# Performance work log

Hardware: AMD Instinct MI355X
Metric: run time of the kernel (lower is better)

Reference implementation:

```python
import jax, jax.numpy as jnp
import numpy as np

EPS = 1e-12  # torch F.normalize eps


def setup_inputs() -> dict:
    key = jax.random.key(0)
    k1, k2, k3 = jax.random.split(key, 3)
    B, way, shot, D, H, W = 64, 5, 1, 640, 5, 5
    nq = 75
    base = jax.random.normal(k1, (B, way, shot, D, H, W), dtype=jnp.float32)
    query = jax.random.normal(k2, (B, nq, D, H, W), dtype=jnp.float32)
    r = jax.random.normal(k3, (2,), dtype=jnp.float32) * 0.1
    return {"base": base, "query": query, "r": r, "neighbor_k": 5}


def reference(base, query, r, neighbor_k):
    B, way, shot, D, H, W = base.shape
    nq = query.shape[1]
    hw = H * W

    # ---- global-cosine branch: spatial-mean descriptors ----
    base_mean = base.reshape(B, way * shot, D, hw).mean(axis=-1)   # [B, way*shot, D]
    query_mean = query.reshape(B, nq, D, hw).mean(axis=-1)         # [B, nq, D]
    bm = base_mean / jnp.maximum(jnp.linalg.norm(base_mean, axis=-1, keepdims=True), EPS)
    qm = query_mean / jnp.maximum(jnp.linalg.norm(query_mean, axis=-1, keepdims=True), EPS)
    logits = jnp.einsum('bqd,bkd->bqk', qm, bm)                    # [B, nq, way*shot]

    # ---- DN4 image-to-class branch (vectorized over the original triple loop) ----
    # query local descriptors: [B, nq, hw, D], L2-normalized over channels
    q = query.reshape(B, nq, D, hw).transpose(0, 1, 3, 2)
    q = q / jnp.linalg.norm(q, axis=-1, keepdims=True)
    # support local descriptors: base_mix [B, way, shot*D, hw], column-normalized
    s = base.reshape(B, way, shot * D, hw)
    s = s / jnp.linalg.norm(s, axis=2, keepdims=True)
    # cosine sims between every query patch and every support patch of each class
    # (requires shot*D == D, i.e. shot == 1, as in the original code)
    sim = jnp.einsum('bqpd,bkdl->bqkpl', q, s)                     # [B, nq, way, hw, hw]
    topk_vals, _ = jax.lax.top_k(sim, neighbor_k)                  # [B, nq, way, hw, k]
    logits_dn4 = topk_vals.sum(axis=(-1, -2)) / neighbor_k         # [B, nq, way]

    return r[0] * logits + r[1] * logits_dn4
```

## Files before the change

### kernel.cpp

```cpp
#include <hip/hip_runtime.h>
#include <hip/hip_bf16.h>
#include <math.h>

#define NB    64
#define WAY   5
#define DCH   640
#define HW    25
#define NQ    75
#define NBK   5
#define EPSN  1e-12f

#define NDG   (DCH / 8)
#define SCOLS 128
#define CD    160
#define NCHK  (DCH / CD)
#define DGC   (CD / 8)
#define CFL   (CD * HW)
#define CTS   132

typedef __attribute__((ext_vector_type(8)))  short  bf16x8;
typedef __attribute__((ext_vector_type(8)))  ushort u16x8;
typedef __attribute__((ext_vector_type(16))) float  f32x16;
typedef __attribute__((ext_vector_type(4)))  float  f32x4;

__device__ inline ushort f2bf(float f) {
    uint u = __float_as_uint(f);
    return (ushort)((u + 0x7FFFu + ((u >> 16) & 1u)) >> 16);
}

__global__ __launch_bounds__(256) void k_prep(const float* __restrict__ base,
                                              float* __restrict__ invs,
                                              float* __restrict__ invsm,
                                              ushort* __restrict__ sT)
{
    const int bk = blockIdx.x;
    const int b  = bk / WAY;
    const int k  = bk - b * WAY;
    const float* src = base + (size_t)bk * (DCH * HW);
    __shared__ float lds[DCH * HW];
    __shared__ float red[256];
    const int tid = threadIdx.x;

    const f32x4* s4 = (const f32x4*)src;
    f32x4* l4 = (f32x4*)lds;
    for (int i = tid; i < (DCH * HW) / 4; i += 256)
        l4[i] = __builtin_nontemporal_load(s4 + i);
    __syncthreads();

    if (tid < HW) {
        float ss = 0.f;
        for (int d = 0; d < DCH; ++d) { float v = lds[d * HW + tid]; ss = fmaf(v, v, ss); }
        invs[bk * HW + tid] = rsqrtf(ss);
    }

    float ssq = 0.f;
    for (int d = tid; d < DCH; d += 256) {
        float s = 0.f;
        #pragma unroll
        for (int pp = 0; pp < HW; ++pp) s += lds[d * HW + pp];
        float m = s * (1.0f / HW);
        ssq = fmaf(m, m, ssq);
    }
    red[tid] = ssq;
    __syncthreads();
    for (int s = 128; s > 0; s >>= 1) {
        if (tid < s) red[tid] += red[tid + s];
        __syncthreads();
    }
    if (tid == 0) invsm[bk] = 1.0f / fmaxf(sqrtf(red[0]), EPSN);

    ushort* dstb = sT + (size_t)b * (NDG * SCOLS * 8);
    for (int t = tid; t < NDG * HW; t += 256) {
        const int dg = t / HW, l = t - dg * HW;
        u16x8 v;
        #pragma unroll
        for (int e = 0; e < 8; ++e) v[e] = f2bf(lds[(dg * 8 + e) * HW + l]);
        *(u16x8*)&dstb[((size_t)dg * SCOLS + k * HW + l) * 8] = v;
    }
    if (k == 0) {
        const u16x8 z = (u16x8)(ushort)0;
        for (int t = tid; t < NDG * 3; t += 256) {
            const int dg = t / 3, sc = 125 + (t - dg * 3);
            *(u16x8*)&dstb[((size_t)dg * SCOLS + sc) * 8] = z;
        }
    }
}

__global__ __launch_bounds__(256, 4) void k_fused(const float* __restrict__ query,
                                                  const ushort* __restrict__ sT,
                                                  const float* __restrict__ invs,
                                                  const float* __restrict__ invsm,
                                                  const float* __restrict__ r,
                                                  float* __restrict__ out)
{
    __shared__ ushort s_bq[2][DGC * 32 * 8];
    __shared__ float invs_l[SCOLS];
    __shared__ float invsm_l[WAY];

    const int tid  = threadIdx.x;
    const int wid  = tid >> 6;
    const int lane = tid & 63;
    const int p    = lane & 31;
    const int hi   = lane >> 5;

    const int wk = (blockIdx.x & 7) * 600 + (blockIdx.x >> 3);
    const int b  = wk / NQ;
    const int q  = wk - b * NQ;

    if (tid < WAY * HW) invs_l[tid] = invs[b * WAY * HW + tid];
    if (tid >= WAY * HW && tid < SCOLS) invs_l[tid] = 0.f;
    if (tid < WAY)      invsm_l[tid] = invsm[b * WAY + tid];

    const float* qrow = query + (size_t)(b * NQ + q) * (DCH * HW);
    const ushort* sTb = sT + (size_t)b * (NDG * SCOLS * 8);

    f32x16 accT = {}, accG = {};
    f32x4 lA0 = {}, lA1 = {}, lA2 = {}, lA3 = {};
    f32x4 lB0 = {}, lB1 = {}, lB2 = {}, lB3 = {};

#define LOADQ(c, R0, R1, R2, R3)                                              \
    {                                                                         \
        const f32x4* s4_ = (const f32x4*)(qrow + (size_t)(c) * CFL);          \
        R0 = __builtin_nontemporal_load(s4_ + tid);                           \
        R1 = __builtin_nontemporal_load(s4_ + 256 + tid);                     \
        R2 = __builtin_nontemporal_load(s4_ + 512 + tid);                     \
        if (tid < 232) R3 = __builtin_nontemporal_load(s4_ + 768 + tid);      \
    }

#define WR4(DST, SLOT, V)                                                     \
    {                                                                         \
        _Pragma("unroll")                                                     \
        for (int j = 0; j < 4; ++j) {                                         \
            const int flat = (SLOT) * 4 + j;                                  \
            const int d  = flat / 25;                                         \
            const int pp = flat - d * 25;                                     \
            (DST)[((d >> 3) * 32 + pp) * 8 + (d & 7)] = f2bf((V)[j]);         \
        }                                                                     \
    }

#define WRITEQ(BUF, R0, R1, R2, R3)                                           \
    {                                                                         \
        ushort* db_ = &s_bq[BUF][0];                                          \
        WR4(db_, tid, R0)                                                     \
        WR4(db_, 256 + tid, R1)                                               \
        WR4(db_, 512 + tid, R2)                                               \
        if (tid < 232) WR4(db_, 768 + tid, R3)                                \
    }

#define COMPUTE(BUF, C)                                                       \
    {                                                                         \
        _Pragma("unroll")                                                     \
        for (int ks = 0; ks < DGC / 2; ++ks) {                                \
            const int dgl = ks * 2 + hi;                                      \
            const bf16x8 bq = *(const bf16x8*)&s_bq[BUF][(dgl * 32 + p) * 8]; \
            const bf16x8 a  = *(const bf16x8*)(sTb +                          \
                ((size_t)((C) * DGC + dgl) * SCOLS + wid * 32 + p) * 8);      \
            accT = __builtin_amdgcn_mfma_f32_32x32x16_bf16(a,  bq, accT, 0, 0, 0); \
            accG = __builtin_amdgcn_mfma_f32_32x32x16_bf16(bq, bq, accG, 0, 0, 0); \
        }                                                                     \
    }

    LOADQ(0, lA0, lA1, lA2, lA3)
    for (int i = tid; i < 2 * DGC * 7; i += 256) {
        const int bu = i / (DGC * 7), r2 = i % (DGC * 7);
        const int dg = r2 / 7, s = r2 % 7;
        *(u16x8*)&s_bq[bu][((dg * 32) + 25 + s) * 8] = (u16x8)(ushort)0;
    }
    WRITEQ(0, lA0, lA1, lA2, lA3)
    __syncthreads();
    LOADQ(1, lB0, lB1, lB2, lB3)
    COMPUTE(0, 0)
    __syncthreads();
    LOADQ(2, lA0, lA1, lA2, lA3)
    WRITEQ(1, lB0, lB1, lB2, lB3)
    __syncthreads();
    COMPUTE(1, 1)
    __syncthreads();
    LOADQ(3, lB0, lB1, lB2, lB3)
    WRITEQ(0, lA0, lA1, lA2, lA3)
    __syncthreads();
    COMPUTE(0, 2)
    __syncthreads();
    WRITEQ(1, lB0, lB1, lB2, lB3)
    __syncthreads();
    COMPUTE(1, 3)

#undef LOADQ
#undef WR4
#undef WRITEQ
#undef COMPUTE

    const bool pok = p < HW;

    float diag = 0.f, qq = 0.f;
    #pragma unroll
    for (int rr = 0; rr < 16; ++rr) {
        const int rowb = (rr & 3) + 8 * (rr >> 2);
        const int row = rowb + 4 * hi;
        diag = (row == p) ? accG[rr] : diag;
        if (row < HW) qq += accG[rr];
    }
    if (!pok) qq = 0.f;
    #pragma unroll
    for (int o = 1; o < 64; o <<= 1) qq += __shfl_xor(qq, o);
    diag += __shfl_xor(diag, 32);
    const float invq = rsqrtf(diag);

    float cs16[16];
    #pragma unroll
    for (int rr = 0; rr < 16; ++rr) {
        float tv = pok ? accT[rr] : 0.f;
        #pragma unroll
        for (int o = 1; o < 32; o <<= 1) tv += __shfl_xor(tv, o);
        cs16[rr] = tv;
    }

    __syncthreads();

    float* ct       = (float*)&s_bq[0][0];
    float* cs_lds   = ct + HW * CTS;
    float* tops_lds = cs_lds + SCOLS;

    if (p == 0) {
        #pragma unroll
        for (int rr = 0; rr < 16; ++rr) {
            const int rowb = (rr & 3) + 8 * (rr >> 2);
            cs_lds[wid * 32 + rowb + 4 * hi] = cs16[rr];
        }
    }
    if (pok) {
        #pragma unroll
        for (int rr = 0; rr < 16; ++rr) {
            const int rowb = (rr & 3) + 8 * (rr >> 2);
            const int scol = wid * 32 + rowb + 4 * hi;
            ct[p * CTS + scol] = accT[rr] * invq * invs_l[scol];
        }
    }
    __syncthreads();

    if (tid < WAY * HW) {
        const int way = tid / HW, pp = tid - way * HW;
        const float* row = &ct[pp * CTS + way * HW];
        float t0 = -3.402823466e38f, t1 = t0, t2 = t0, t3 = t0, t4 = t0;
        #pragma unroll
        for (int j = 0; j < HW; ++j) {
            float x = row[j], a;
            a = fmaxf(t0, x); x = fminf(t0, x); t0 = a;
            a = fmaxf(t1, x); x = fminf(t1, x); t1 = a;
            a = fmaxf(t2, x); x = fminf(t2, x); t2 = a;
            a = fmaxf(t3, x); x = fminf(t3, x); t3 = a;
            a = fmaxf(t4, x); x = fminf(t4, x); t4 = a;
        }
        tops_lds[tid] = t0 + t1 + t2 + t3 + t4;
    }
    __syncthreads();

    if (tid < WAY) {
        float gsv = 0.f, dn = 0.f;
        #pragma unroll
        for (int j = 0; j < HW; ++j) {
            gsv += cs_lds[tid * HW + j];
            dn  += tops_lds[tid * HW + j];
        }
        const float invqm = 1.0f / fmaxf(sqrtf(qq) * (1.0f / HW), EPSN);
        out[(size_t)(b * NQ + q) * WAY + tid] =
            r[0] * gsv * (1.0f / 625.0f) * invqm * invsm_l[tid]
          + r[1] * dn * (1.0f / NBK);
    }
}

extern "C" void kernel_launch(void* const* d_in, const int* in_sizes, int n_in,
                              void* d_out, int out_size, void* d_ws, size_t ws_size,
                              hipStream_t stream)
{
    const float* base  = (const float*)d_in[0];
    const float* query = (const float*)d_in[1];
    const float* r     = (const float*)d_in[2];
    float* out = (float*)d_out;

    float* invs   = (float*)d_ws;
    float* invsm  = invs + NB * WAY * HW;
    ushort* sT    = (ushort*)((float*)d_ws + 16384);

    k_prep<<<NB * WAY, 256, 0, stream>>>(base, invs, invsm, sT);
    k_fused<<<NB * NQ, 256, 0, stream>>>(query, sT, invs, invsm, r, out);
}
```

Measured before the change: 119.0 us.

## Stream query chunks via global_load_lds into a 4-deep pipeline and preload support fragments

```diff
diff --git a/kernel.cpp b/kernel.cpp
--- a/kernel.cpp
+++ b/kernel.cpp
@@ -12,10 +12,10 @@
 
 #define NDG   (DCH / 8)
 #define SCOLS 128
-#define CD    160
+#define CD    64
 #define NCHK  (DCH / CD)
-#define DGC   (CD / 8)
 #define CFL   (CD * HW)
+#define QTR   (CFL / 4)
 #define CTS   132
 
 typedef __attribute__((ext_vector_type(8)))  short  bf16x8;
@@ -86,14 +86,15 @@
     }
 }
 
-__global__ __launch_bounds__(256, 4) void k_fused(const float* __restrict__ query,
+__global__ __launch_bounds__(256, 2) void k_fused(const float* __restrict__ query,
                                                   const ushort* __restrict__ sT,
                                                   const float* __restrict__ invs,
                                                   const float* __restrict__ invsm,
                                                   const float* __restrict__ r,
                                                   float* __restrict__ out)
 {
-    __shared__ ushort s_bq[2][DGC * 32 * 8];
+    __shared__ __align__(16) float  f_lds[4][CFL];
+    __shared__ __align__(16) ushort b_lds[2][8 * 32 * 8];
     __shared__ float invs_l[SCOLS];
     __shared__ float invsm_l[WAY];
 
@@ -102,6 +103,9 @@
     const int lane = tid & 63;
     const int p    = lane & 31;
     const int hi   = lane >> 5;
+    const int dgl  = tid >> 5;
+    const int pt   = tid & 31;
+    const int pct  = (pt < HW) ? pt : (HW - 1);
 
     const int wk = (blockIdx.x & 7) * 600 + (blockIdx.x >> 3);
     const int b  = wk / NQ;
@@ -114,81 +118,77 @@
     const float* qrow = query + (size_t)(b * NQ + q) * (DCH * HW);
     const ushort* sTb = sT + (size_t)b * (NDG * SCOLS * 8);
 
+    bf16x8 Afr[40];
+    #pragma unroll
+    for (int s = 0; s < 40; ++s) {
+        const int dg = s * 2 + hi;
+        Afr[s] = *(const bf16x8*)(sTb + ((size_t)dg * SCOLS + wid * 32 + p) * 8);
+    }
+
     f32x16 accT = {}, accG = {};
-    f32x4 lA0 = {}, lA1 = {}, lA2 = {}, lA3 = {};
-    f32x4 lB0 = {}, lB1 = {}, lB2 = {}, lB3 = {};
-
-#define LOADQ(c, R0, R1, R2, R3)                                              \
-    {                                                                         \
-        const f32x4* s4_ = (const f32x4*)(qrow + (size_t)(c) * CFL);          \
-        R0 = __builtin_nontemporal_load(s4_ + tid);                           \
-        R1 = __builtin_nontemporal_load(s4_ + 256 + tid);                     \
-        R2 = __builtin_nontemporal_load(s4_ + 512 + tid);                     \
-        if (tid < 232) R3 = __builtin_nontemporal_load(s4_ + 768 + tid);      \
-    }
-
-#define WR4(DST, SLOT, V)                                                     \
-    {                                                                         \
-        _Pragma("unroll")                                                     \
-        for (int j = 0; j < 4; ++j) {                                         \
-            const int flat = (SLOT) * 4 + j;                                  \
-            const int d  = flat / 25;                                         \
-            const int pp = flat - d * 25;                                     \
-            (DST)[((d >> 3) * 32 + pp) * 8 + (d & 7)] = f2bf((V)[j]);         \
-        }                                                                     \
-    }
-
-#define WRITEQ(BUF, R0, R1, R2, R3)                                           \
-    {                                                                         \
-        ushort* db_ = &s_bq[BUF][0];                                          \
-        WR4(db_, tid, R0)                                                     \
-        WR4(db_, 256 + tid, R1)                                               \
-        WR4(db_, 512 + tid, R2)                                               \
-        if (tid < 232) WR4(db_, 768 + tid, R3)                                \
-    }
-
-#define COMPUTE(BUF, C)                                                       \
-    {                                                                         \
-        _Pragma("unroll")                                                     \
-        for (int ks = 0; ks < DGC / 2; ++ks) {                                \
-            const int dgl = ks * 2 + hi;                                      \
-            const bf16x8 bq = *(const bf16x8*)&s_bq[BUF][(dgl * 32 + p) * 8]; \
-            const bf16x8 a  = *(const bf16x8*)(sTb +                          \
-                ((size_t)((C) * DGC + dgl) * SCOLS + wid * 32 + p) * 8);      \
-            accT = __builtin_amdgcn_mfma_f32_32x32x16_bf16(a,  bq, accT, 0, 0, 0); \
+
+#define ISSUE(cc)                                                              \
+    {                                                                          \
+        const float* s_ = qrow + (cc) * CFL + wid * QTR;                       \
+        float* d_ = &f_lds[(cc) & 3][wid * QTR];                               \
+        __builtin_amdgcn_global_load_lds(                                      \
+            (const __attribute__((address_space(1))) uint*)(s_ + lane * 4),    \
+            (__attribute__((address_space(3))) uint*)d_, 16, 0, 0);            \
+        if (lane < 36)                                                         \
+            __builtin_amdgcn_global_load_lds(                                  \
+                (const __attribute__((address_space(1))) uint*)(s_ + 256 + lane * 4), \
+                (__attribute__((address_space(3))) uint*)(d_ + 256), 16, 0, 0); \
+    }
+
+#define TRANSPOSE(cc)                                                          \
+    {                                                                          \
+        const float* fs_ = &f_lds[(cc) & 3][dgl * 200];                        \
+        u16x8 tv_;                                                             \
+        _Pragma("unroll")                                                      \
+        for (int e = 0; e < 8; ++e) tv_[e] = f2bf(fs_[e * HW + pct]);          \
+        *(u16x8*)&b_lds[(cc) & 1][(dgl * 32 + pt) * 8] = tv_;                  \
+    }
+
+#define COMPUTE(cc)                                                            \
+    {                                                                          \
+        _Pragma("unroll")                                                      \
+        for (int ks = 0; ks < 4; ++ks) {                                       \
+            const bf16x8 bq = *(const bf16x8*)&b_lds[(cc) & 1][((ks * 2 + hi) * 32 + p) * 8]; \
+            accT = __builtin_amdgcn_mfma_f32_32x32x16_bf16(Afr[(cc) * 4 + ks], bq, accT, 0, 0, 0); \
             accG = __builtin_amdgcn_mfma_f32_32x32x16_bf16(bq, bq, accG, 0, 0, 0); \
-        }                                                                     \
-    }
-
-    LOADQ(0, lA0, lA1, lA2, lA3)
-    for (int i = tid; i < 2 * DGC * 7; i += 256) {
-        const int bu = i / (DGC * 7), r2 = i % (DGC * 7);
-        const int dg = r2 / 7, s = r2 % 7;
-        *(u16x8*)&s_bq[bu][((dg * 32) + 25 + s) * 8] = (u16x8)(ushort)0;
-    }
-    WRITEQ(0, lA0, lA1, lA2, lA3)
-    __syncthreads();
-    LOADQ(1, lB0, lB1, lB2, lB3)
-    COMPUTE(0, 0)
-    __syncthreads();
-    LOADQ(2, lA0, lA1, lA2, lA3)
-    WRITEQ(1, lB0, lB1, lB2, lB3)
-    __syncthreads();
-    COMPUTE(1, 1)
-    __syncthreads();
-    LOADQ(3, lB0, lB1, lB2, lB3)
-    WRITEQ(0, lA0, lA1, lA2, lA3)
-    __syncthreads();
-    COMPUTE(0, 2)
-    __syncthreads();
-    WRITEQ(1, lB0, lB1, lB2, lB3)
-    __syncthreads();
-    COMPUTE(1, 3)
-
-#undef LOADQ
-#undef WR4
-#undef WRITEQ
+        }                                                                      \
+    }
+
+#define LG0 asm volatile("s_waitcnt lgkmcnt(0)" ::: "memory");
+#define VM4 asm volatile("s_waitcnt vmcnt(4)" ::: "memory");
+#define VM2 asm volatile("s_waitcnt vmcnt(2)" ::: "memory");
+#define VM0 asm volatile("s_waitcnt vmcnt(0)" ::: "memory");
+#define BAR __builtin_amdgcn_s_barrier(); __builtin_amdgcn_sched_barrier(0);
+
+    ISSUE(0) ISSUE(1) ISSUE(2) ISSUE(3)
+    asm volatile("s_waitcnt vmcnt(6)" ::: "memory");
+    __builtin_amdgcn_sched_barrier(0);
+    TRANSPOSE(0)
+
+    LG0 VM4 BAR TRANSPOSE(1) ISSUE(4) COMPUTE(0)
+    LG0 VM4 BAR TRANSPOSE(2) ISSUE(5) COMPUTE(1)
+    LG0 VM4 BAR TRANSPOSE(3) ISSUE(6) COMPUTE(2)
+    LG0 VM4 BAR TRANSPOSE(4) ISSUE(7) COMPUTE(3)
+    LG0 VM4 BAR TRANSPOSE(5) ISSUE(8) COMPUTE(4)
+    LG0 VM4 BAR TRANSPOSE(6) ISSUE(9) COMPUTE(5)
+    LG0 VM4 BAR TRANSPOSE(7)          COMPUTE(6)
+    LG0 VM2 BAR TRANSPOSE(8)          COMPUTE(7)
+    LG0 VM0 BAR TRANSPOSE(9)          COMPUTE(8)
+    LG0     BAR                       COMPUTE(9)
+
+#undef ISSUE
+#undef TRANSPOSE
 #undef COMPUTE
+#undef LG0
+#undef VM4
+#undef VM2
+#undef VM0
+#undef BAR
 
     const bool pok = p < HW;
 
@@ -217,7 +217,7 @@
 
     __syncthreads();
 
-    float* ct       = (float*)&s_bq[0][0];
+    float* ct       = &f_lds[0][0];
     float* cs_lds   = ct + HW * CTS;
     float* tops_lds = cs_lds + SCOLS;
 
```

New measurement: 142.6 us. 19.9% more time.
